# Kernel optimization log

Measured on AMD Instinct MI355X. Metric: run time of the kernel, lower is better.

Reference implementation:

```python
import jax, jax.numpy as jnp
import numpy as np

B = 64        # number of graphs in the batch
NPG = 1024    # nodes per graph (uniform batch_num_nodes)
N = B * NPG   # total nodes = 65536
D = 512       # input feature dim
DEG = 32      # average degree
K = 0.5       # keep-percent
DROP = NPG - int(np.ceil(K * NPG))  # number of lowest-score nodes zeroed per graph


def setup_inputs() -> dict:
    key = jax.random.key(0)
    k1, k2, k3, k4 = jax.random.split(key, 4)
    features = jax.random.normal(k1, (N, D), dtype=jnp.float32)
    # edges constrained inside each graph's node block (batched DGL graph is block-diagonal)
    offsets = (jnp.arange(B, dtype=jnp.int64) * NPG)[:, None]
    src = (jax.random.randint(k2, (B, NPG * DEG), 0, NPG, dtype=jnp.int64) + offsets).reshape(-1)
    dst = (jax.random.randint(k3, (B, NPG * DEG), 0, NPG, dtype=jnp.int64) + offsets).reshape(-1)
    # GraphConv(input_dim=D, out=1) parameters (glorot-ish scale)
    weight = jax.random.normal(k4, (D, 1), dtype=jnp.float32) * (1.0 / np.sqrt(D))
    bias = jnp.zeros((1,), dtype=jnp.float32)
    return {"features": features, "src": src, "dst": dst, "weight": weight, "bias": bias}


def reference(features, src, dst, weight, bias):
    # --- GraphConv(D -> 1, norm=True, bias=True, activation=relu) ---
    # old-DGL norm=True: symmetric normalization with in-degrees, norm=deg^-0.5 (0 for isolated)
    deg = jnp.zeros((N,), features.dtype).at[dst].add(1.0)
    norm = jnp.where(deg > 0, deg ** -0.5, 0.0)[:, None]          # [N,1]
    # in_feats > out_feats: project first, then aggregate scalars
    h = (features @ weight) * norm                                # [N,1]
    agg = jnp.zeros_like(h).at[dst].add(h[src])                   # sum over in-edges
    w = jax.nn.relu(agg * norm + bias)                            # [N,1] scores
    # --- per-graph top-k masking: zero the DROP smallest scores in each graph ---
    wb = w.reshape(B, NPG)
    ranks = jnp.argsort(jnp.argsort(wb, axis=1), axis=1)          # rank 0 = smallest
    wb = jnp.where(ranks < DROP, jnp.zeros((), wb.dtype), wb)
    # --- elementwise gating of features by (masked) scores ---
    return features * wb.reshape(N, 1)
```

## Files before the change

kernel.cpp:

```cpp
#include <hip/hip_runtime.h>

#define NTOT 65536
#define DIM  512
#define BGR  64
#define NPG  1024
#define DROPN 512
#define SLICES 8
#define DEG_BLOCKS 64
#define MV_BLOCKS 2048

typedef float vf4 __attribute__((ext_vector_type(4)));
typedef unsigned long long u64;

__global__ __launch_bounds__(256) void k1_matvec_deg(
        const float* __restrict__ X, const float* __restrict__ W,
        const int* __restrict__ dst,
        float* __restrict__ p, float* __restrict__ norm,
        float* __restrict__ agg, int* __restrict__ ticket, int epg) {
    __shared__ int dl[NPG];
    if (blockIdx.x < DEG_BLOCKS) {
        const int g = blockIdx.x;
        const int nbase = g * NPG;
        for (int i = threadIdx.x; i < NPG; i += 256) dl[i] = 0;
        ((vf4*)(agg + nbase))[threadIdx.x] = (vf4){0.f, 0.f, 0.f, 0.f};
        if (threadIdx.x == 0) ticket[g] = 0;
        __syncthreads();
        const int4* d4 = (const int4*)(dst + (size_t)g * epg);
        const int n4 = epg >> 2;
        for (int i = threadIdx.x; i < n4; i += 256) {
            int4 d = d4[i];
            atomicAdd(&dl[d.x - nbase], 1);
            atomicAdd(&dl[d.y - nbase], 1);
            atomicAdd(&dl[d.z - nbase], 1);
            atomicAdd(&dl[d.w - nbase], 1);
        }
        __syncthreads();
        for (int i = threadIdx.x; i < NPG; i += 256) {
            int d = dl[i];
            norm[nbase + i] = d > 0 ? rsqrtf((float)d) : 0.f;
        }
    } else {
        const int lane = threadIdx.x & 63;
        const int wid  = ((blockIdx.x - DEG_BLOCKS) * 256 + threadIdx.x) >> 6;
        const int nw   = (MV_BLOCKS * 256) >> 6;
        const vf4* wr = (const vf4*)W;
        const vf4 w0 = wr[lane], w1 = wr[lane + 64];
        for (int row = wid; row < NTOT; row += 2 * nw) {
            const int row2 = row + nw;
            const vf4* xr0 = (const vf4*)(X + (size_t)row  * DIM);
            const vf4* xr1 = (const vf4*)(X + (size_t)row2 * DIM);
            vf4 a0 = xr0[lane], a1 = xr0[lane + 64];
            vf4 b0 = xr1[lane], b1 = xr1[lane + 64];
            vf4 m0 = a0 * w0 + a1 * w1;
            vf4 m1 = b0 * w0 + b1 * w1;
            float s0 = m0[0] + m0[1] + m0[2] + m0[3];
            float s1 = m1[0] + m1[1] + m1[2] + m1[3];
            #pragma unroll
            for (int off = 32; off > 0; off >>= 1) {
                s0 += __shfl_down(s0, off, 64);
                s1 += __shfl_down(s1, off, 64);
            }
            if (lane == 0) { p[row] = s0; p[row2] = s1; }
        }
    }
}

__global__ __launch_bounds__(256) void k2_agg_topk(
        const int* __restrict__ src, const int* __restrict__ dst,
        const float* __restrict__ p, const float* __restrict__ norm,
        const float* __restrict__ bias,
        float* __restrict__ agg, int* __restrict__ ticket,
        float* __restrict__ gate, int epg) {
    __shared__ float hl[NPG];
    __shared__ float al[NPG];
    __shared__ unsigned int hist[256];
    __shared__ unsigned int selbin, selkp;
    __shared__ unsigned int wsum[4];
    __shared__ int lastFlag;
    const int b = blockIdx.x;
    const int g = b & (BGR - 1);
    const int slice = b >> 6;
    const int nbase = g * NPG;
    const int eps = epg / SLICES;
    const int t = threadIdx.x;
    {
        const vf4* pv = (const vf4*)(p + nbase);
        const vf4* nv = (const vf4*)(norm + nbase);
        ((vf4*)hl)[t] = pv[t] * nv[t];
        ((vf4*)al)[t] = (vf4){0.f, 0.f, 0.f, 0.f};
    }
    __syncthreads();
    const int4* s4 = (const int4*)(src + (size_t)g * epg + (size_t)slice * eps);
    const int4* d4 = (const int4*)(dst + (size_t)g * epg + (size_t)slice * eps);
    const int n4 = eps >> 2;
    for (int i = t; i < n4; i += 256) {
        int4 s = s4[i];
        int4 d = d4[i];
        atomicAdd(&al[d.x - nbase], hl[s.x - nbase]);
        atomicAdd(&al[d.y - nbase], hl[s.y - nbase]);
        atomicAdd(&al[d.z - nbase], hl[s.z - nbase]);
        atomicAdd(&al[d.w - nbase], hl[s.w - nbase]);
    }
    __syncthreads();
    #pragma unroll
    for (int c = 0; c < 4; c++) {
        int i = t + 256 * c;
        atomicAdd(&agg[nbase + i], al[i]);
    }
    __threadfence();
    if (t == 0) lastFlag = (atomicAdd(&ticket[g], 1) == SLICES - 1);
    __syncthreads();
    if (!lastFlag) return;
    __threadfence();
    const float bb = bias[0];
    float w[4];
    unsigned int v[4];
    bool act[4];
    const vf4* nv = (const vf4*)(norm + nbase);
    vf4 nrm4 = nv[t];
    #pragma unroll
    for (int c = 0; c < 4; c++) {
        int i = 4 * t + c;
        float a = atomicAdd(&agg[nbase + i], 0.f);
        float ww = a * nrm4[c] + bb;
        ww = ww > 0.f ? ww : 0.f;
        w[c] = ww;
        v[c] = __float_as_uint(ww);
        act[c] = true;
    }
    unsigned int kp = DROPN;
    unsigned int T = 0;
    const int lane = t & 63;
    const int wv   = t >> 6;
    #pragma unroll
    for (int shift = 24; shift >= 0; shift -= 8) {
        hist[t] = 0;
        __syncthreads();
        #pragma unroll
        for (int c = 0; c < 4; c++)
            if (act[c]) atomicAdd(&hist[(v[c] >> shift) & 255u], 1u);
        __syncthreads();
        if (t < 64) {
            unsigned int h0 = hist[t*4], h1 = hist[t*4+1], h2 = hist[t*4+2], h3 = hist[t*4+3];
            unsigned int lsum = h0 + h1 + h2 + h3;
            unsigned int x = lsum;
            #pragma unroll
            for (int off = 1; off < 64; off <<= 1) {
                unsigned int y = (unsigned int)__shfl_up((int)x, off, 64);
                if (lane >= off) x += y;
            }
            unsigned int excl = x - lsum;
            hist[t*4]   = excl + h0;
            hist[t*4+1] = excl + h0 + h1;
            hist[t*4+2] = excl + h0 + h1 + h2;
            hist[t*4+3] = excl + h0 + h1 + h2 + h3;
        }
        __syncthreads();
        {
            unsigned int lo = (t == 0) ? 0u : hist[t-1];
            unsigned int hi = hist[t];
            if (lo <= kp && kp < hi) { selbin = (unsigned int)t; selkp = kp - lo; }
        }
        __syncthreads();
        const unsigned int sb = selbin;
        kp = selkp;
        #pragma unroll
        for (int c = 0; c < 4; c++)
            act[c] = act[c] && (((v[c] >> shift) & 255u) == sb);
        T |= sb << shift;
    }
    int cnt = 0;
    int pre[4];
    #pragma unroll
    for (int c = 0; c < 4; c++) { pre[c] = cnt; cnt += act[c] ? 1 : 0; }
    int x = cnt;
    #pragma unroll
    for (int off = 1; off < 64; off <<= 1) {
        int y = __shfl_up(x, off, 64);
        if (lane >= off) x += y;
    }
    if (lane == 63) wsum[wv] = (unsigned int)x;
    __syncthreads();
    int base = 0;
    for (int i = 0; i < wv; i++) base += (int)wsum[i];
    const int excl = base + x - cnt;
    vf4 gout;
    #pragma unroll
    for (int c = 0; c < 4; c++) {
        bool keep = act[c] ? ((unsigned int)(excl + pre[c]) >= kp) : (v[c] > T);
        gout[c] = keep ? w[c] : 0.f;
    }
    ((vf4*)(gate + nbase))[t] = gout;
}

__global__ __launch_bounds__(256) void k3_gate(
        const float* __restrict__ X, const float* __restrict__ gate,
        float* __restrict__ out) {
    const int lane = threadIdx.x & 63;
    const int nw   = (gridDim.x * blockDim.x) >> 6;
    const int wid  = (blockIdx.x * blockDim.x + threadIdx.x) >> 6;
    for (int row = wid; row < NTOT; row += nw) {
        float g = gate[row];
        vf4* o = (vf4*)(out + (size_t)row * DIM);
        if (g == 0.f) {
            vf4 z = (vf4){0.f, 0.f, 0.f, 0.f};
            __builtin_nontemporal_store(z, &o[lane]);
            __builtin_nontemporal_store(z, &o[lane + 64]);
        } else {
            const vf4* xr = (const vf4*)(X + (size_t)row * DIM);
            vf4 a = xr[lane] * g;
            vf4 c = xr[lane + 64] * g;
            __builtin_nontemporal_store(a, &o[lane]);
            __builtin_nontemporal_store(c, &o[lane + 64]);
        }
    }
}

extern "C" void kernel_launch(void* const* d_in, const int* in_sizes, int n_in,
                              void* d_out, int out_size, void* d_ws, size_t ws_size,
                              hipStream_t stream) {
    const float* X    = (const float*)d_in[0];
    const int*   src  = (const int*)d_in[1];
    const int*   dst  = (const int*)d_in[2];
    const float* W    = (const float*)d_in[3];
    const float* bias = (const float*)d_in[4];
    float* out = (float*)d_out;
    int E   = in_sizes[1];
    int epg = E / BGR;

    float* ws     = (float*)d_ws;
    float* p      = ws;
    float* norm   = ws + 1 * NTOT;
    float* gate   = ws + 2 * NTOT;
    float* agg    = ws + 3 * NTOT;
    int*   ticket = (int*)(ws + 4 * NTOT);

    k1_matvec_deg<<<DEG_BLOCKS + MV_BLOCKS, 256, 0, stream>>>(X, W, dst, p, norm, agg, ticket, epg);
    k2_agg_topk<<<BGR * SLICES, 256, 0, stream>>>(src, dst, p, norm, bias, agg, ticket, gate, epg);
    k3_gate<<<2048, 256, 0, stream>>>(X, gate, out);
}
```

Measured before the change: 306.9 us.

## Replace atomic ticket reduction with per-slice partials and fuse top-k selection into gating

The aggregation kernel now writes per-slice partial sums to separate workspace buffers, so the global float atomics, threadfences and last-block ticket are gone. A new kernel launches 32 blocks per graph. Each block reduces the 8 partials, redundantly runs the radix top-k selection for its graph, keeps the gate in shared memory and scales its 32 rows of features. This drops the separate gate kernel and the gate round trip through memory. In exchange the selection work is repeated 32 times per graph and the workspace for partials grows.

After: 279.3 us. 1.1x faster.

```diff
diff --git a/kernel.cpp b/kernel.cpp
--- a/kernel.cpp
+++ b/kernel.cpp
@@ -8,6 +8,7 @@
 #define SLICES 8
 #define DEG_BLOCKS 64
 #define MV_BLOCKS 2048
+#define GPB 32
 
 typedef float vf4 __attribute__((ext_vector_type(4)));
 typedef unsigned long long u64;
@@ -15,15 +16,12 @@
 __global__ __launch_bounds__(256) void k1_matvec_deg(
         const float* __restrict__ X, const float* __restrict__ W,
         const int* __restrict__ dst,
-        float* __restrict__ p, float* __restrict__ norm,
-        float* __restrict__ agg, int* __restrict__ ticket, int epg) {
+        float* __restrict__ p, float* __restrict__ norm, int epg) {
     __shared__ int dl[NPG];
     if (blockIdx.x < DEG_BLOCKS) {
         const int g = blockIdx.x;
         const int nbase = g * NPG;
         for (int i = threadIdx.x; i < NPG; i += 256) dl[i] = 0;
-        ((vf4*)(agg + nbase))[threadIdx.x] = (vf4){0.f, 0.f, 0.f, 0.f};
-        if (threadIdx.x == 0) ticket[g] = 0;
         __syncthreads();
         const int4* d4 = (const int4*)(dst + (size_t)g * epg);
         const int n4 = epg >> 2;
@@ -65,35 +63,26 @@
     }
 }
 
-__global__ __launch_bounds__(256) void k2_agg_topk(
+__global__ __launch_bounds__(256) void k2_agg(
         const int* __restrict__ src, const int* __restrict__ dst,
         const float* __restrict__ p, const float* __restrict__ norm,
-        const float* __restrict__ bias,
-        float* __restrict__ agg, int* __restrict__ ticket,
-        float* __restrict__ gate, int epg) {
+        float* __restrict__ agg_part, int epg) {
     __shared__ float hl[NPG];
     __shared__ float al[NPG];
-    __shared__ unsigned int hist[256];
-    __shared__ unsigned int selbin, selkp;
-    __shared__ unsigned int wsum[4];
-    __shared__ int lastFlag;
     const int b = blockIdx.x;
     const int g = b & (BGR - 1);
     const int slice = b >> 6;
     const int nbase = g * NPG;
     const int eps = epg / SLICES;
-    const int t = threadIdx.x;
-    {
-        const vf4* pv = (const vf4*)(p + nbase);
-        const vf4* nv = (const vf4*)(norm + nbase);
-        ((vf4*)hl)[t] = pv[t] * nv[t];
-        ((vf4*)al)[t] = (vf4){0.f, 0.f, 0.f, 0.f};
+    for (int i = threadIdx.x; i < NPG; i += 256) {
+        hl[i] = p[nbase + i] * norm[nbase + i];
+        al[i] = 0.f;
     }
     __syncthreads();
     const int4* s4 = (const int4*)(src + (size_t)g * epg + (size_t)slice * eps);
     const int4* d4 = (const int4*)(dst + (size_t)g * epg + (size_t)slice * eps);
     const int n4 = eps >> 2;
-    for (int i = t; i < n4; i += 256) {
+    for (int i = threadIdx.x; i < n4; i += 256) {
         int4 s = s4[i];
         int4 d = d4[i];
         atomicAdd(&al[d.x - nbase], hl[s.x - nbase]);
@@ -102,27 +91,37 @@
         atomicAdd(&al[d.w - nbase], hl[s.w - nbase]);
     }
     __syncthreads();
-    #pragma unroll
-    for (int c = 0; c < 4; c++) {
-        int i = t + 256 * c;
-        atomicAdd(&agg[nbase + i], al[i]);
-    }
-    __threadfence();
-    if (t == 0) lastFlag = (atomicAdd(&ticket[g], 1) == SLICES - 1);
-    __syncthreads();
-    if (!lastFlag) return;
-    __threadfence();
+    float* op = agg_part + (size_t)slice * NTOT + nbase;
+    for (int i = threadIdx.x; i < NPG; i += 256) op[i] = al[i];
+}
+
+__global__ __launch_bounds__(256) void k34_select_gate(
+        const float* __restrict__ agg_part, const float* __restrict__ norm,
+        const float* __restrict__ bias, const float* __restrict__ X,
+        float* __restrict__ out) {
+    __shared__ unsigned int hist[256];
+    __shared__ unsigned int selbin, selkp;
+    __shared__ unsigned int wsum[4];
+    __shared__ float gw[NPG];
+    const int b = blockIdx.x;
+    const int g   = b >> 5;
+    const int sub = b & (GPB - 1);
+    const int t = threadIdx.x;
+    const int lane = t & 63;
+    const int wv   = t >> 6;
+    const int nbase = g * NPG;
     const float bb = bias[0];
     float w[4];
     unsigned int v[4];
     bool act[4];
-    const vf4* nv = (const vf4*)(norm + nbase);
-    vf4 nrm4 = nv[t];
+    vf4 nrm4 = ((const vf4*)(norm + nbase))[t];
+    vf4 a4 = (vf4){0.f, 0.f, 0.f, 0.f};
+    #pragma unroll
+    for (int s = 0; s < SLICES; s++)
+        a4 += ((const vf4*)(agg_part + (size_t)s * NTOT + nbase))[t];
     #pragma unroll
     for (int c = 0; c < 4; c++) {
-        int i = 4 * t + c;
-        float a = atomicAdd(&agg[nbase + i], 0.f);
-        float ww = a * nrm4[c] + bb;
+        float ww = a4[c] * nrm4[c] + bb;
         ww = ww > 0.f ? ww : 0.f;
         w[c] = ww;
         v[c] = __float_as_uint(ww);
@@ -130,8 +129,6 @@
     }
     unsigned int kp = DROPN;
     unsigned int T = 0;
-    const int lane = t & 63;
-    const int wv   = t >> 6;
     #pragma unroll
     for (int shift = 24; shift >= 0; shift -= 8) {
         hist[t] = 0;
@@ -184,34 +181,26 @@
     int base = 0;
     for (int i = 0; i < wv; i++) base += (int)wsum[i];
     const int excl = base + x - cnt;
-    vf4 gout;
     #pragma unroll
     for (int c = 0; c < 4; c++) {
         bool keep = act[c] ? ((unsigned int)(excl + pre[c]) >= kp) : (v[c] > T);
-        gout[c] = keep ? w[c] : 0.f;
-    }
-    ((vf4*)(gate + nbase))[t] = gout;
-}
-
-__global__ __launch_bounds__(256) void k3_gate(
-        const float* __restrict__ X, const float* __restrict__ gate,
-        float* __restrict__ out) {
-    const int lane = threadIdx.x & 63;
-    const int nw   = (gridDim.x * blockDim.x) >> 6;
-    const int wid  = (blockIdx.x * blockDim.x + threadIdx.x) >> 6;
-    for (int row = wid; row < NTOT; row += nw) {
-        float g = gate[row];
+        gw[4*t + c] = keep ? w[c] : 0.f;
+    }
+    __syncthreads();
+    for (int r = wv; r < 32; r += 4) {
+        const int row = nbase + sub * 32 + r;
+        const float gv = gw[sub * 32 + r];
         vf4* o = (vf4*)(out + (size_t)row * DIM);
-        if (g == 0.f) {
+        if (gv == 0.f) {
             vf4 z = (vf4){0.f, 0.f, 0.f, 0.f};
             __builtin_nontemporal_store(z, &o[lane]);
             __builtin_nontemporal_store(z, &o[lane + 64]);
         } else {
             const vf4* xr = (const vf4*)(X + (size_t)row * DIM);
-            vf4 a = xr[lane] * g;
-            vf4 c = xr[lane + 64] * g;
+            vf4 a = xr[lane] * gv;
+            vf4 c2 = xr[lane + 64] * gv;
             __builtin_nontemporal_store(a, &o[lane]);
-            __builtin_nontemporal_store(c, &o[lane + 64]);
+            __builtin_nontemporal_store(c2, &o[lane + 64]);
         }
     }
 }
@@ -228,14 +217,12 @@
     int E   = in_sizes[1];
     int epg = E / BGR;
 
-    float* ws     = (float*)d_ws;
-    float* p      = ws;
-    float* norm   = ws + 1 * NTOT;
-    float* gate   = ws + 2 * NTOT;
-    float* agg    = ws + 3 * NTOT;
-    int*   ticket = (int*)(ws + 4 * NTOT);
-
-    k1_matvec_deg<<<DEG_BLOCKS + MV_BLOCKS, 256, 0, stream>>>(X, W, dst, p, norm, agg, ticket, epg);
-    k2_agg_topk<<<BGR * SLICES, 256, 0, stream>>>(src, dst, p, norm, bias, agg, ticket, gate, epg);
-    k3_gate<<<2048, 256, 0, stream>>>(X, gate, out);
-}
+    float* ws       = (float*)d_ws;
+    float* p        = ws;
+    float* norm     = ws + 1 * NTOT;
+    float* agg_part = ws + 2 * NTOT;
+
+    k1_matvec_deg<<<DEG_BLOCKS + MV_BLOCKS, 256, 0, stream>>>(X, W, dst, p, norm, epg);
+    k2_agg<<<BGR * SLICES, 256, 0, stream>>>(src, dst, p, norm, agg_part, epg);
+    k34_select_gate<<<BGR * GPB, 256, 0, stream>>>(agg_part, norm, bias, X, out);
+}
```
